# Performance work log

Hardware: AMD Instinct MI355X
Metric: run time of the kernel (lower is better)

## Reference

```python
import jax, jax.numpy as jnp
import numpy as np

C = 256   # d_model
L = 2     # num_decoder_layers
B = 4
H = 128
W = 128
WH = 8    # dec_win_h
WW = 16   # dec_win_w
EPS = 1e-5


def _gn(x, w, b):
    # GroupNorm with 1 group: normalize over (C,H,W) per sample, per-channel affine
    mu = jnp.mean(x, axis=(1, 2, 3), keepdims=True)
    var = jnp.mean((x - mu) ** 2, axis=(1, 2, 3), keepdims=True)
    xn = (x - mu) * jax.lax.rsqrt(var + EPS)
    return xn * w[:, None, None] + b[:, None, None]


def _conv1x1(x, w, b):
    # x: [B,C,H,W], w: [O,C], b: [O]
    return jnp.einsum('bchw,oc->bohw', x, w) + b[:, None, None]


def _avgpool3(x):
    # AvgPool2d(3, stride=1, padding=1, count_include_pad=False)
    dims = (1, 1, 3, 3)
    strides = (1, 1, 1, 1)
    pad = [(0, 0), (0, 0), (1, 1), (1, 1)]
    s = jax.lax.reduce_window(x, 0.0, jax.lax.add, dims, strides, pad)
    ones = jnp.ones((1, 1) + x.shape[2:], x.dtype)
    cnt = jax.lax.reduce_window(ones, 0.0, jax.lax.add, dims, strides, pad)
    return s / cnt


def _mix(x):
    # PoolFormer token mixer: avgpool(x) - x
    return _avgpool3(x) - x


def _win_part(x, wh, ww):
    # [B,C,H,W] -> [B*nWin, C, wh, ww]
    b, c, h, w = x.shape
    x = x.reshape(b, c, h // wh, wh, w // ww, ww)
    x = x.transpose(0, 2, 4, 1, 3, 5)
    return x.reshape(-1, c, wh, ww)


def _agp(tgt, mem, qw, qb, kw, kb, vw, vb):
    # AttentionGuidedPooling; NOTE: torch uses .view(B,-1,C) on [B,C,H,W],
    # a raw reshape (not a transpose) -- replicated faithfully here.
    bw, c, h, w = mem.shape
    n = h * w
    q = _conv1x1(tgt, qw, qb).reshape(bw, n, c)
    k = _conv1x1(mem, kw, kb).reshape(bw, n, c)
    v = _conv1x1(mem, vw, vb).reshape(bw, n, c)
    attn = jax.nn.softmax(jnp.einsum('bnc,bmc->bnm', q, k), axis=-1)
    out = jnp.einsum('bnm,bmc->bnc', attn, v)
    return out.reshape(bw, c, h, w)


def _layer(tgt, mem, p):
    (gn1_w, gn1_b, gn2_w, gn2_b, ls1, ls2, ls3,
     qw, qb, kw, kb, vw, vb, fc1_w, fc1_b, fc2_w, fc2_b) = p
    tgt2 = tgt + ls1[:, None, None] * _mix(_gn(tgt, gn1_w, gn1_b))
    guided = _agp(tgt, mem, qw, qb, kw, kb, vw, vb)
    tgt3 = tgt2 + guided
    tgt3 = tgt2 + ls2[:, None, None] * _mix(_gn(tgt3, gn1_w, gn1_b))
    h = _gn(tgt3, gn2_w, gn2_b)
    h = _conv1x1(h, fc1_w, fc1_b)
    h = jax.nn.gelu(h, approximate=False)  # torch nn.GELU default (erf)
    h = _conv1x1(h, fc2_w, fc2_b)
    return tgt3 + ls3[:, None, None] * h


def setup_inputs() -> dict:
    key = jax.random.key(0)
    ks = jax.random.split(key, 16)
    s = 0.02
    inp = {
        'src': jax.random.normal(ks[0], (B, C, H, W), jnp.float32),
        'query_feats': jax.random.normal(ks[1], (B, C, H, W), jnp.float32),
        'gn1_w': jnp.ones((L, C), jnp.float32),
        'gn1_b': jnp.zeros((L, C), jnp.float32),
        'gn2_w': jnp.ones((L, C), jnp.float32),
        'gn2_b': jnp.zeros((L, C), jnp.float32),
        'ls1': 1e-5 * jnp.ones((L, C), jnp.float32),
        'ls2': 1e-5 * jnp.ones((L, C), jnp.float32),
        'ls3': 1e-5 * jnp.ones((L, C), jnp.float32),
        'qw': s * jax.random.normal(ks[2], (L, C, C), jnp.float32),
        'qb': jnp.zeros((L, C), jnp.float32),
        'kw': s * jax.random.normal(ks[3], (L, C, C), jnp.float32),
        'kb': jnp.zeros((L, C), jnp.float32),
        'vw': s * jax.random.normal(ks[4], (L, C, C), jnp.float32),
        'vb': jnp.zeros((L, C), jnp.float32),
        'fc1_w': s * jax.random.normal(ks[5], (L, 2 * C, C), jnp.float32),
        'fc1_b': jnp.zeros((L, 2 * C), jnp.float32),
        'fc2_w': s * jax.random.normal(ks[6], (L, C, 2 * C), jnp.float32),
        'fc2_b': jnp.zeros((L, C), jnp.float32),
        'gnf_w': jnp.ones((C,), jnp.float32),
        'gnf_b': jnp.zeros((C,), jnp.float32),
    }
    return inp


def reference(src, query_feats, gn1_w, gn1_b, gn2_w, gn2_b, ls1, ls2, ls3,
              qw, qb, kw, kb, vw, vb, fc1_w, fc1_b, fc2_w, fc2_b, gnf_w, gnf_b):
    # pq_stride=8 -> div_ratio=1: memory windows same size as tgt windows
    mem = _win_part(src, WH, WW)
    out = _win_part(query_feats, WH, WW)
    for l in range(L):
        p = (gn1_w[l], gn1_b[l], gn2_w[l], gn2_b[l], ls1[l], ls2[l], ls3[l],
             qw[l], qb[l], kw[l], kb[l], vw[l], vb[l],
             fc1_w[l], fc1_b[l], fc2_w[l], fc2_b[l])
        out = _layer(out, mem, p)
    out = _gn(out, gnf_w, gnf_b)
    # window reverse -> [B, C, H, W] -> sequence [B, H*W, C]
    nwh, nww = H // WH, W // WW
    x = out.reshape(B, nwh, nww, C, WH, WW).transpose(0, 3, 1, 4, 2, 5)
    x = x.reshape(B, C, H * W)
    hs = jnp.swapaxes(x, 1, 2)[None]        # [1, B, N, C]
    return jnp.swapaxes(hs, 1, 2)           # [1, N, B, C]
```

## Files before the change

### kernel.cpp

```cpp
#include <hip/hip_runtime.h>
#include <hip/hip_bf16.h>

typedef __hip_bfloat16 bf16_t;
typedef short bf16x8 __attribute__((ext_vector_type(8)));
typedef float f32x4 __attribute__((ext_vector_type(4)));

__device__ __forceinline__ float bfr(unsigned short u) {
  return __uint_as_float(((unsigned int)u) << 16);
}
__device__ __forceinline__ float b2f(bf16_t h) { return __bfloat162float(h); }
__device__ __forceinline__ bf16_t f2b(float f) { return __float2bfloat16(f); }
__device__ __forceinline__ unsigned short f2bu(float f) {
  union { bf16_t h; unsigned short u; } cv; cv.h = __float2bfloat16(f); return cv.u;
}
__device__ __forceinline__ void unpk2(unsigned int u, float& a, float& b) {
  a = __uint_as_float(u << 16);
  b = __uint_as_float(u & 0xffff0000u);
}
__device__ __forceinline__ void ld8b(const bf16_t* p, float* o) {
  uint4 v = *(const uint4*)p;
  unpk2(v.x,o[0],o[1]); unpk2(v.y,o[2],o[3]); unpk2(v.z,o[4],o[5]); unpk2(v.w,o[6],o[7]);
}
__device__ __forceinline__ void unpk8(uint4 v, float* o) {
  unpk2(v.x,o[0],o[1]); unpk2(v.y,o[2],o[3]); unpk2(v.z,o[4],o[5]); unpk2(v.w,o[6],o[7]);
}
__device__ __forceinline__ int flag_of(const void* w) {
  return (*(const unsigned int*)w == 0x3F803F80u) ? 0 : 1;
}

typedef __attribute__((address_space(3))) void lds_t;
typedef __attribute__((address_space(1))) void glb_t;
__device__ __forceinline__ void gll16(const void* g, void* l) {
  __builtin_amdgcn_global_load_lds((glb_t*)g, (lds_t*)l, 16, 0, 0);
}

struct Srcs { const void* p[18]; };

__global__ __launch_bounds__(256)
void k_cvtall(Srcs a, bf16_t* __restrict__ PR) {
  const int ck = blockIdx.x*256 + threadIdx.x;
  if (ck >= 115520) return;
  constexpr int N8[18]  = {64,64,64,64,64,64,64,64,64,128,64,32,32,16384,16384,16384,32768,32768};
  constexpr int DOF[18] = {0,512,1024,1536,2048,2560,3072,3584,4096,4608,5632,6144,6400,8192,139264,270336,401408,663552};
  int s = 0, base = 0, doff = 0, cum = 0;
#pragma unroll
  for (int i = 0; i < 17; ++i) {
    cum += N8[i];
    if (ck >= cum) { s = i + 1; base = cum; doff = DOF[i + 1]; }
  }
  const int o8 = ck - base;
  const void* sp = a.p[s];
  const int fl = flag_of(a.p[0]);
  uint4 w;
  if (fl) {
    const float4* f = (const float4*)sp;
    float4 v0 = f[o8*2], v1 = f[o8*2+1];
    w.x = ((unsigned)f2bu(v0.y)<<16) | f2bu(v0.x);
    w.y = ((unsigned)f2bu(v0.w)<<16) | f2bu(v0.z);
    w.z = ((unsigned)f2bu(v1.y)<<16) | f2bu(v1.x);
    w.w = ((unsigned)f2bu(v1.w)<<16) | f2bu(v1.z);
  } else {
    w = ((const uint4*)sp)[o8];
  }
  *(uint4*)(PR + doff + o8*8) = w;
}

__global__ __launch_bounds__(256)
void k_xt2(const void* __restrict__ inA, bf16_t* __restrict__ outA,
           const void* __restrict__ inB, bf16_t* __restrict__ outB,
           const void* __restrict__ flagw) {
  __shared__ unsigned short L[128*130];
  const void* in = blockIdx.z ? inB : inA;
  bf16_t* out = blockIdx.z ? outB : outA;
  const int win = blockIdx.x, tile = blockIdx.y, tid = threadIdx.x;
  const int IC = tile << 7;
  const int fl = flag_of(flagw);
  const int b = win >> 7, whi = (win >> 3) & 15, wwi = win & 7;

  for (int i = 0; i < 8; ++i) {
    int idx = tid + (i<<8);
    int r = idx >> 4, ch = idx & 15;
    unsigned int w0, w1, w2, w3;
    int c = IC + r;
    int hq = ch >> 1, wq = (ch & 1) << 3;
    long gaddr = ((long)((b<<8) + c) << 14) + ((whi<<3) + hq)*128 + (wwi<<4) + wq;
    if (fl) {
      const float* gp = (const float*)in + gaddr;
      float4 aa = *(const float4*)gp, bb = *(const float4*)(gp+4);
      w0 = ((unsigned)f2bu(aa.y)<<16)|f2bu(aa.x); w1 = ((unsigned)f2bu(aa.w)<<16)|f2bu(aa.z);
      w2 = ((unsigned)f2bu(bb.y)<<16)|f2bu(bb.x); w3 = ((unsigned)f2bu(bb.w)<<16)|f2bu(bb.z);
    } else {
      uint4 v = *(const uint4*)((const bf16_t*)in + gaddr);
      w0 = v.x; w1 = v.y; w2 = v.z; w3 = v.w;
    }
    unsigned int* Lp = (unsigned int*)L;
    int u32o = (r*130 + (ch<<3)) >> 1;
    Lp[u32o+0] = w0; Lp[u32o+1] = w1; Lp[u32o+2] = w2; Lp[u32o+3] = w3;
  }
  __syncthreads();
  for (int i = 0; i < 8; ++i) {
    int idx = tid + (i<<8);
    int q = idx >> 4, ch = idx & 15;
    unsigned short pk[8];
#pragma unroll
    for (int j = 0; j < 8; ++j) pk[j] = L[((ch<<3) + j)*130 + q];
    *(uint4*)(out + (long)win*32768 + (long)q*256 + IC + (ch<<3)) = *(uint4*)pk;
  }
}

__global__ __launch_bounds__(256) void k_statsP(const bf16_t* __restrict__ X, float* __restrict__ st) {
  __shared__ float s1[256], s2[256];
  int w = blockIdx.x, tid = threadIdx.x;
  const bf16_t* x = X + ((long)w << 15);
  float a = 0.f, b = 0.f;
  for (int i = tid*8; i < 32768; i += 2048) {
    float t[8]; ld8b(x + i, t);
#pragma unroll
    for (int j = 0; j < 8; ++j) { a += t[j]; b += t[j]*t[j]; }
  }
  s1[tid] = a; s2[tid] = b;
  __syncthreads();
  for (int off = 128; off > 0; off >>= 1) {
    if (tid < off) { s1[tid] += s1[tid+off]; s2[tid] += s2[tid+off]; }
    __syncthreads();
  }
  if (tid == 0) {
    float mu = s1[0] * (1.0f/32768.0f);
    float var = s2[0] * (1.0f/32768.0f) - mu*mu;
    st[(w<<1)]   = mu;
    st[(w<<1)+1] = rsqrtf(var + 1e-5f);
  }
}

template<int GATH, int GN2>
__global__ __launch_bounds__(512, 4)
void k_poolf(const bf16_t* __restrict__ Xp, const bf16_t* __restrict__ Gc,
             bf16_t* __restrict__ Out,
             const bf16_t* __restrict__ lsv, const bf16_t* __restrict__ gw,
             bf16_t* __restrict__ G2,
             const bf16_t* __restrict__ g2w, const bf16_t* __restrict__ g2b) {
  __shared__ unsigned short L[32768];
  __shared__ float s1[8], s2[8];
  __shared__ float mr[2];
  const int win = blockIdx.x;
  const int tid = threadIdx.x;
  const long wb = (long)win << 15;
  float a = 0.f, b = 0.f;

#pragma unroll
  for (int i = 0; i < 8; ++i) {
    int k = (i<<9) + tid;
    int p = k >> 5, c8 = k & 31;
    uint4 v = *(const uint4*)(Xp + wb + (p<<8) + (c8<<3));
    *(uint4*)&L[(p<<8) + ((c8 ^ ((p>>3)&7))<<3)] = v;
    if (!GATH) {
      float t[8]; unpk8(v, t);
#pragma unroll
      for (int j = 0; j < 8; ++j) { a += t[j]; b += t[j]*t[j]; }
    }
  }
  if (GATH) {
    __syncthreads();
#pragma unroll
    for (int i = 0; i < 8; ++i) {
      int k = (i<<9) + tid;
      int c = k >> 4, p0 = (k & 15) << 3;
      uint4 gv = *(const uint4*)(Gc + wb + (c<<7) + p0);
      float g[8]; unpk8(gv, g);
      int ch = c >> 3, cl = c & 7;
      int sl = ((ch ^ ((p0>>3) & 7))<<3) + cl;
#pragma unroll
      for (int j = 0; j < 8; ++j) {
        int idx = ((p0 + j)<<8) + sl;
        float xx = bfr(L[idx]) + g[j];
        a += xx; b += xx*xx;
        L[idx] = f2bu(xx);
      }
    }
  }
#pragma unroll
  for (int d = 1; d < 64; d <<= 1) { a += __shfl_xor(a, d); b += __shfl_xor(b, d); }
  if ((tid & 63) == 0) { s1[tid>>6] = a; s2[tid>>6] = b; }
  __syncthreads();
  if (tid == 0) {
    float sa = 0.f, sb = 0.f;
#pragma unroll
    for (int i = 0; i < 8; ++i) { sa += s1[i]; sb += s2[i]; }
    float mu = sa * (1.0f/32768.0f);
    float var = sb * (1.0f/32768.0f) - mu*mu;
    mr[0] = mu; mr[1] = rsqrtf(var + 1e-5f);
  }
  __syncthreads();
  const float rstd = mr[1];
  const int c = tid & 255;
  const int hb = (tid >> 8) << 2;
  const int ch = c >> 3, cl = c & 7;
  const float scl = b2f(lsv[c]) * b2f(gw[c]) * rstd;
  float oa = 0.f, ob = 0.f;

  float rm1[16], r0[16], rp1[16];
#pragma unroll
  for (int ww = 0; ww < 16; ++ww) {
    int p0_ = (hb<<4) + ww;
    r0[ww] = bfr(L[(p0_<<8) + ((ch ^ ((p0_>>3)&7))<<3) + cl]);
    int p1_ = ((hb+1)<<4) + ww;
    rp1[ww] = bfr(L[(p1_<<8) + ((ch ^ ((p1_>>3)&7))<<3) + cl]);
  }
  if (hb > 0) {
#pragma unroll
    for (int ww = 0; ww < 16; ++ww) {
      int pm = ((hb-1)<<4) + ww;
      rm1[ww] = bfr(L[(pm<<8) + ((ch ^ ((pm>>3)&7))<<3) + cl]);
    }
  }
#pragma unroll
  for (int hl = 0; hl < 4; ++hl) {
    int h = hb + hl;
    float cs[16];
    float hc = 1.f + (h > 0 ? 1.f : 0.f) + (h < 7 ? 1.f : 0.f);
#pragma unroll
    for (int ww = 0; ww < 16; ++ww)
      cs[ww] = r0[ww] + (h > 0 ? rm1[ww] : 0.f) + (h < 7 ? rp1[ww] : 0.f);
#pragma unroll
    for (int ww = 0; ww < 16; ++ww) {
      float s = cs[ww];
      float wc = 1.f;
      if (ww > 0)  { s += cs[ww-1]; wc += 1.f; }
      if (ww < 15) { s += cs[ww+1]; wc += 1.f; }
      float avg = s / (hc * wc);
      float xx = r0[ww];
      int p = (h<<4) + ww;
      float base = xx;
      if (GATH) base = bfr(*(const unsigned short*)(Xp + wb + (p<<8) + c));
      float val = base + scl * (avg - xx);
      if (GN2) { oa += val; ob += val*val; }
      Out[wb + (p<<8) + c] = f2b(val);
    }
#pragma unroll
    for (int ww = 0; ww < 16; ++ww) { rm1[ww] = r0[ww]; r0[ww] = rp1[ww]; }
    if (hl < 3 && (h + 2) <= 7) {
      int hp = (h+2) << 4;
#pragma unroll
      for (int ww = 0; ww < 16; ++ww) {
        int p = hp + ww;
        rp1[ww] = bfr(L[(p<<8) + ((ch ^ ((p>>3)&7))<<3) + cl]);
      }
    }
  }
  if (GN2) {
#pragma unroll
    for (int d = 1; d < 64; d <<= 1) { oa += __shfl_xor(oa, d); ob += __shfl_xor(ob, d); }
    if ((tid & 63) == 0) { s1[tid>>6] = oa; s2[tid>>6] = ob; }
    __syncthreads();
    if (tid == 0) {
      float sa = 0.f, sb = 0.f;
#pragma unroll
      for (int i = 0; i < 8; ++i) { sa += s1[i]; sb += s2[i]; }
      float mu = sa * (1.0f/32768.0f);
      float var = sb * (1.0f/32768.0f) - mu*mu;
      mr[0] = mu; mr[1] = rsqrtf(var + 1e-5f);
    }
    __syncthreads();
    const float mu2 = mr[0], rs2 = mr[1];
#pragma unroll
    for (int i = 0; i < 8; ++i) {
      int k = (i<<9) + tid;
      int p = k >> 5, cv = k & 31;
      uint4 v = *(const uint4*)(Out + wb + (p<<8) + (cv<<3));
      float t[8]; unpk8(v, t);
      uint4 wv = *(const uint4*)(g2w + (cv<<3));
      uint4 bv = *(const uint4*)(g2b + (cv<<3));
      float wf[8], bf2[8]; unpk8(wv, wf); unpk8(bv, bf2);
      unsigned short pk[8];
#pragma unroll
      for (int j = 0; j < 8; ++j) pk[j] = f2bu((t[j]-mu2)*rs2*wf[j] + bf2[j]);
      *(uint4*)(G2 + wb + (p<<8) + (cv<<3)) = *(uint4*)pk;
    }
  }
}

#define GM_QKV  0
#define GM_NM   1
#define GM_GELU 2
#define GM_RES  3

template<int MODE>
__global__ __launch_bounds__(256, 2)
void k_gemm(const bf16_t* __restrict__ A, long sA, int lda,
            const bf16_t* __restrict__ B0, const bf16_t* __restrict__ B1,
            long sB, int ldb,
            bf16_t* __restrict__ Y, long sY, int ldy,
            const bf16_t* __restrict__ bias,
            const bf16_t* __restrict__ res, long sR,
            const bf16_t* __restrict__ ls,
            int K) {
  __shared__ uint4 LB[2048];
  unsigned short* As = (unsigned short*)LB;
  unsigned short* Bs = (unsigned short*)LB + 8192;
  unsigned short* E  = (unsigned short*)LB;
  const int win = blockIdx.x;
  const int tid = threadIdx.x;
  const int w = tid >> 6, lane = tid & 63;
  const int l15 = lane & 15, quad = lane >> 4;
  const int m0w = (w >> 1) << 6, n0w = (w & 1) << 6;

  int sel = 0, m0;
  const bf16_t *Ab, *Bb; bf16_t* Yb; const bf16_t* biasb = nullptr;
  if (MODE == GM_QKV) {
    sel = blockIdx.y >> 1; m0 = (blockIdx.y & 1) << 7;
    Ab = A + sel*131072 + (long)m0*lda;
    Bb = (sel ? B1 : B0) + (long)win*sB;
    Yb = Y + (long)sel*16777216 + (long)win*sY;
    biasb = bias + sel*512 + m0;
  } else {
    m0 = blockIdx.y << 7;
    Ab = A + (long)win*sA + (long)m0*lda;
    Bb = B0 + (long)win*sB;
    Yb = Y + (long)win*sY;
    if (bias) biasb = bias + m0;
  }
  const bool CT = (MODE == GM_QKV) && (sel < 2);

  int rr_[4], co_[4], lo_[4];
#pragma unroll
  for (int j = 0; j < 4; ++j) {
    int ck = (j<<8) + (w<<6) + lane;
    int r = ck >> 3;
    rr_[j] = r;
    co_[j] = ((ck & 7) ^ (r & 7)) << 3;
    lo_[j] = ((j<<8) + (w<<6)) << 3;
  }

  f32x4 acc[4][4];
#pragma unroll
  for (int i = 0; i < 4; ++i)
#pragma unroll
    for (int j = 0; j < 4; ++j) acc[i][j] = (f32x4){0.f,0.f,0.f,0.f};

  for (int k0 = 0; k0 < K; k0 += 64) {
#pragma unroll
    for (int j = 0; j < 4; ++j) {
      gll16(Ab + (long)rr_[j]*lda + k0 + co_[j], As + lo_[j]);
      gll16(Bb + (long)rr_[j]*ldb + k0 + co_[j], Bs + lo_[j]);
    }
    __syncthreads();
#pragma unroll
    for (int kk = 0; kk < 2; ++kk) {
      bf16x8 af[4], bv[4];
#pragma unroll
      for (int im = 0; im < 4; ++im) {
        int R = m0w + (im<<4) + l15;
        af[im] = *(const bf16x8*)&As[(R<<6) + ((((kk<<2)+quad) ^ (R&7))<<3)];
      }
#pragma unroll
      for (int in = 0; in < 4; ++in) {
        int R = n0w + (in<<4) + l15;
        bv[in] = *(const bf16x8*)&Bs[(R<<6) + ((((kk<<2)+quad) ^ (R&7))<<3)];
      }
      if (CT) {
#pragma unroll
        for (int im = 0; im < 4; ++im)
#pragma unroll
          for (int in = 0; in < 4; ++in)
            acc[im][in] = __builtin_amdgcn_mfma_f32_16x16x32_bf16(bv[in], af[im], acc[im][in], 0, 0, 0);
      } else {
#pragma unroll
        for (int im = 0; im < 4; ++im)
#pragma unroll
          for (int in = 0; in < 4; ++in)
            acc[im][in] = __builtin_amdgcn_mfma_f32_16x16x32_bf16(af[im], bv[in], acc[im][in], 0, 0, 0);
      }
    }
    __syncthreads();
  }

  if (MODE == GM_QKV && sel == 2) {
#pragma unroll
    for (int im = 0; im < 4; ++im) {
#pragma unroll
      for (int in = 0; in < 4; ++in) {
        f32x4 v = acc[im][in];
        int tok = n0w + (in<<4) + l15;
        int c0 = m0w + (im<<4) + (quad<<2);
        int u0 = c0 >> 1;
        float x0 = v[0] + b2f(biasb[c0]);
        float x1 = v[1] + b2f(biasb[c0+1]);
        float x2 = v[2] + b2f(biasb[c0+2]);
        float x3 = v[3] + b2f(biasb[c0+3]);
        int sl = (((u0>>3) ^ (tok&7))<<3) + (u0&7);
        *(unsigned int*)&E[(tok<<6) + sl]       = (unsigned)f2bu(x0) | ((unsigned)f2bu(x2)<<16);
        *(unsigned int*)&E[((128+tok)<<6) + sl] = (unsigned)f2bu(x1) | ((unsigned)f2bu(x3)<<16);
      }
    }
    __syncthreads();
#pragma unroll
    for (int i = 0; i < 8; ++i) {
      int ck = (i<<8) + tid;
      int cp = ck >> 3, u8 = ck & 7;
      uint4 v = *(const uint4*)&E[(cp<<6) + ((u8 ^ (cp&7))<<3)];
      *(uint4*)(Yb + (long)cp*128 + (m0>>1) + (u8<<3)) = v;
    }
    return;
  }

  if (CT) {
#pragma unroll
    for (int half = 0; half < 2; ++half) {
      if (m0w == (half<<6)) {
#pragma unroll
        for (int im = 0; im < 4; ++im) {
          int row = (im<<4) + l15;
          float bm = b2f(biasb[(half<<6) + row]);
#pragma unroll
          for (int in = 0; in < 4; ++in) {
            f32x4 v = acc[im][in];
            unsigned short pk[4];
#pragma unroll
            for (int r = 0; r < 4; ++r) pk[r] = f2bu(v[r] + bm);
            *(ushort4*)&E[row*136 + n0w + (in<<4) + (quad<<2)] = *(ushort4*)pk;
          }
        }
      }
      __syncthreads();
#pragma unroll
      for (int i = 0; i < 4; ++i) {
        int ck = (i<<8) + tid;
        int row = ck >> 4, c8 = (ck & 15) << 3;
        uint4 v = *(const uint4*)&E[row*136 + c8];
        *(uint4*)(Yb + (long)(m0 + (half<<6) + row)*ldy + c8) = v;
      }
      __syncthreads();
    }
    return;
  }

#pragma unroll
  for (int half = 0; half < 2; ++half) {
    if (n0w == (half<<6)) {
#pragma unroll
      for (int in = 0; in < 4; ++in) {
        int row = (in<<4) + l15;
#pragma unroll
        for (int im = 0; im < 4; ++im) {
          f32x4 v = acc[im][in];
          int mb = m0w + (im<<4) + (quad<<2);
          unsigned short pk[4];
#pragma unroll
          for (int r = 0; r < 4; ++r) {
            float x = v[r];
            if (MODE == GM_GELU || MODE == GM_RES) x += b2f(biasb[mb + r]);
            if (MODE == GM_GELU) x = 0.5f * x * (1.0f + erff(x * 0.70710678118654752f));
            pk[r] = f2bu(x);
          }
          *(ushort4*)&E[row*136 + mb] = *(ushort4*)pk;
        }
      }
    }
    __syncthreads();
#pragma unroll
    for (int i = 0; i < 4; ++i) {
      int ck = (i<<8) + tid;
      int rloc = ck >> 4, c8 = (ck & 15) << 3;
      long oadr = (long)((half<<6) + rloc)*ldy + m0 + c8;
      uint4 v = *(const uint4*)&E[rloc*136 + c8];
      if (MODE == GM_RES) {
        float t[8]; unpk8(v, t);
        uint4 rv = *(const uint4*)(res + (long)win*sR + oadr);
        float rf[8]; unpk8(rv, rf);
        uint4 lv = *(const uint4*)(ls + m0 + c8);
        float lf[8]; unpk8(lv, lf);
        unsigned short pk[8];
#pragma unroll
        for (int j = 0; j < 8; ++j) pk[j] = f2bu(rf[j] + lf[j]*t[j]);
        *(uint4*)(Yb + oadr) = *(uint4*)pk;
      } else {
        *(uint4*)(Yb + oadr) = v;
      }
    }
    __syncthreads();
  }
}

__global__ __launch_bounds__(256, 2)
void k_scores(const bf16_t* __restrict__ Kc, const bf16_t* __restrict__ Qc,
              bf16_t* __restrict__ P) {
  __shared__ uint4 LB[2048];
  __shared__ float red[2][2][128];
  unsigned short* As = (unsigned short*)LB;
  unsigned short* Bs = (unsigned short*)LB + 8192;
  const int win = blockIdx.x;
  const int tid = threadIdx.x;
  const int w = tid >> 6, lane = tid & 63;
  const int l15 = lane & 15, quad = lane >> 4;
  const int m0w = (w >> 1) << 6, n0w = (w & 1) << 6;
  const int wrow = w >> 1;
  const bf16_t* Ab = Kc + ((long)win << 15);
  const bf16_t* Bb = Qc + ((long)win << 15);

  int rr_[4], co_[4], lo_[4];
#pragma unroll
  for (int j = 0; j < 4; ++j) {
    int ck = (j<<8) + (w<<6) + lane;
    int r = ck >> 3;
    rr_[j] = r;
    co_[j] = ((ck & 7) ^ (r & 7)) << 3;
    lo_[j] = ((j<<8) + (w<<6)) << 3;
  }

  f32x4 acc[4][4];
#pragma unroll
  for (int i = 0; i < 4; ++i)
#pragma unroll
    for (int j = 0; j < 4; ++j) acc[i][j] = (f32x4){0.f,0.f,0.f,0.f};

  for (int k0 = 0; k0 < 256; k0 += 64) {
#pragma unroll
    for (int j = 0; j < 4; ++j) {
      gll16(Ab + (long)rr_[j]*256 + k0 + co_[j], As + lo_[j]);
      gll16(Bb + (long)rr_[j]*256 + k0 + co_[j], Bs + lo_[j]);
    }
    __syncthreads();
#pragma unroll
    for (int kk = 0; kk < 2; ++kk) {
      bf16x8 af[4], bv[4];
#pragma unroll
      for (int im = 0; im < 4; ++im) {
        int R = m0w + (im<<4) + l15;
        af[im] = *(const bf16x8*)&As[(R<<6) + ((((kk<<2)+quad) ^ (R&7))<<3)];
      }
#pragma unroll
      for (int in = 0; in < 4; ++in) {
        int R = n0w + (in<<4) + l15;
        bv[in] = *(const bf16x8*)&Bs[(R<<6) + ((((kk<<2)+quad) ^ (R&7))<<3)];
      }
#pragma unroll
      for (int im = 0; im < 4; ++im)
#pragma unroll
        for (int in = 0; in < 4; ++in)
          acc[im][in] = __builtin_amdgcn_mfma_f32_16x16x32_bf16(af[im], bv[in], acc[im][in], 0, 0, 0);
    }
    __syncthreads();
  }

  float mx[4];
#pragma unroll
  for (int in = 0; in < 4; ++in) {
    float m = -3.4e38f;
#pragma unroll
    for (int im = 0; im < 4; ++im)
#pragma unroll
      for (int r = 0; r < 4; ++r) m = fmaxf(m, acc[im][in][r]);
    m = fmaxf(m, __shfl_xor(m, 16));
    m = fmaxf(m, __shfl_xor(m, 32));
    mx[in] = m;
  }
  if (quad == 0) {
#pragma unroll
    for (int in = 0; in < 4; ++in) red[0][wrow][n0w + (in<<4) + l15] = mx[in];
  }
  __syncthreads();
  float fm[4];
#pragma unroll
  for (int in = 0; in < 4; ++in) {
    int t = n0w + (in<<4) + l15;
    fm[in] = fmaxf(red[0][0][t], red[0][1][t]);
  }
  float sm[4];
#pragma unroll
  for (int in = 0; in < 4; ++in) {
    float s = 0.f;
#pragma unroll
    for (int im = 0; im < 4; ++im)
#pragma unroll
      for (int r = 0; r < 4; ++r) {
        float e = __expf(acc[im][in][r] - fm[in]);
        acc[im][in][r] = e;
        s += e;
      }
    s += __shfl_xor(s, 16);
    s += __shfl_xor(s, 32);
    sm[in] = s;
  }
  if (quad == 0) {
#pragma unroll
    for (int in = 0; in < 4; ++in) red[1][wrow][n0w + (in<<4) + l15] = sm[in];
  }
  __syncthreads();
  bf16_t* Pw = P + ((long)win << 14);
#pragma unroll
  for (int in = 0; in < 4; ++in) {
    int t = n0w + (in<<4) + l15;
    float inv = 1.0f / (red[1][0][t] + red[1][1][t]);
#pragma unroll
    for (int im = 0; im < 4; ++im) {
      int u = m0w + (im<<4) + (quad<<2);
      unsigned short pk[4];
#pragma unroll
      for (int r = 0; r < 4; ++r) pk[r] = f2bu(acc[im][in][r] * inv);
      *(ushort4*)(Pw + t*128 + u) = *(ushort4*)pk;
    }
  }
}

__global__ __launch_bounds__(256)
void k_final(const bf16_t* __restrict__ Tp, const float* __restrict__ st,
             const bf16_t* __restrict__ gw, const bf16_t* __restrict__ gb,
             void* __restrict__ out, const void* __restrict__ flagw) {
  const int fl = flag_of(flagw);
  long k = (long)blockIdx.x*256 + threadIdx.x;
  int c8 = (int)(k & 31), p = (int)((k >> 5) & 127), win = (int)(k >> 12);
  float mu = st[win*2], rs = st[win*2+1];
  uint4 v = *(const uint4*)(Tp + (k<<3));
  float t[8]; unpk8(v, t);
  uint4 wv = *(const uint4*)(gw + (c8<<3));
  uint4 bv = *(const uint4*)(gb + (c8<<3));
  float wf[8], bf2[8]; unpk8(wv, wf); unpk8(bv, bf2);
  float o_[8];
#pragma unroll
  for (int j = 0; j < 8; ++j) o_[j] = (t[j] - mu) * rs * wf[j] + bf2[j];
  int b = win >> 7, whi = (win >> 3) & 15, wwi = win & 7;
  int n = ((whi<<3) + (p>>4)) * 128 + (wwi<<4) + (p & 15);
  long o = ((long)((n<<2) + b) << 8) + (c8<<3);
  if (fl) {
    float4 f0, f1;
    f0.x=o_[0]; f0.y=o_[1]; f0.z=o_[2]; f0.w=o_[3];
    f1.x=o_[4]; f1.y=o_[5]; f1.z=o_[6]; f1.w=o_[7];
    *(float4*)((float*)out + o)     = f0;
    *(float4*)((float*)out + o + 4) = f1;
  } else {
    unsigned short pk[8];
#pragma unroll
    for (int j = 0; j < 8; ++j) pk[j] = f2bu(o_[j]);
    *(uint4*)((bf16_t*)out + o) = *(uint4*)pk;
  }
}

extern "C" void kernel_launch(void* const* d_in, const int* in_sizes, int n_in,
                              void* d_out, int out_size, void* d_ws, size_t ws_size,
                              hipStream_t stream) {
  (void)in_sizes; (void)n_in; (void)out_size; (void)ws_size;
  const void* src   = d_in[0];
  const void* qfeat = d_in[1];

  bf16_t* W    = (bf16_t*)d_ws;
  bf16_t* Tp   = W;
  bf16_t* T2p  = W + 16777216;
  bf16_t* Sp   = W + 33554432;
  bf16_t* slA  = W + 50331648;
  bf16_t* KcGc = W + 67108864;
  bf16_t* Vc   = W + 83886080;
  bf16_t* Hp   = KcGc;
  bf16_t* P    = W + 100663296;
  bf16_t* PR   = W + 109051904;
  float*  ST   = (float*)(W + 110100480);
  float*  st0  = ST;

  bf16_t* gn1w = PR;
  bf16_t* gn2w = PR + 512;
  bf16_t* gn2b = PR + 1024;
  bf16_t* ls1  = PR + 1536;
  bf16_t* ls2  = PR + 2048;
  bf16_t* ls3  = PR + 2560;
  bf16_t* qb   = PR + 3072;
  bf16_t* f1b  = PR + 4608;
  bf16_t* f2bp = PR + 5632;
  bf16_t* gfw  = PR + 6144;
  bf16_t* gfb  = PR + 6400;
  bf16_t* qw   = PR + 8192;
  bf16_t* f1w  = PR + 401408;
  bf16_t* f2w  = PR + 663552;

  Srcs sa;
  const int map[18] = {2,4,5,6,7,8,10,12,14,16,18,19,20,9,11,13,15,17};
  for (int i = 0; i < 18; ++i) sa.p[i] = d_in[map[i]];
  k_cvtall<<<452, 256, 0, stream>>>(sa, PR);

  k_xt2<<<dim3(512,2,2), 256, 0, stream>>>(qfeat, Tp, src, Sp, d_in[2]);

  for (int l = 0; l < 2; ++l) {
    k_poolf<0,0><<<512, 512, 0, stream>>>(Tp, nullptr, T2p, ls1 + l*256, gn1w + l*256,
                                          nullptr, nullptr, nullptr);
    k_gemm<GM_QKV><<<dim3(512,6), 256, 0, stream>>>(
        qw + l*65536, 0, 256, Tp, Sp, 32768, 256, slA, 32768, 128,
        qb + l*256, nullptr, 0, nullptr, 256);
    k_scores<<<512, 256, 0, stream>>>(KcGc, slA, P);
    k_gemm<GM_NM><<<dim3(512,2), 256, 0, stream>>>(
        Vc, 32768, 128, P, nullptr, 16384, 128, KcGc, 32768, 256,
        nullptr, nullptr, 0, nullptr, 128);
    k_poolf<1,1><<<512, 512, 0, stream>>>(T2p, KcGc, Tp, ls2 + l*256, gn1w + l*256,
                                          slA, gn2w + l*256, gn2b + l*256);
    k_gemm<GM_GELU><<<dim3(512,4), 256, 0, stream>>>(
        f1w + l*131072, 0, 256, slA, nullptr, 32768, 256, Hp, 65536, 512,
        f1b + l*512, nullptr, 0, nullptr, 256);
    k_gemm<GM_RES><<<dim3(512,2), 256, 0, stream>>>(
        f2w + l*131072, 0, 512, Hp, nullptr, 65536, 512, Tp, 32768, 256,
        f2bp + l*256, Tp, 32768, ls3 + l*256, 512);
  }

  k_statsP<<<512, 256, 0, stream>>>(Tp, st0);
  k_final<<<8192, 256, 0, stream>>>(Tp, st0, gfw, gfb, d_out, d_in[2]);
}
```

Baseline: 739.7 us.

## Fuse final GroupNorm stats into last residual GEMM and restructure window transpose

Removes the separate k_statsP pass by having the last FC2 residual GEMM accumulate per-window sum and sum-of-squares with atomics, with k_final deriving mean and rstd from them. The stats buffer is zeroed inside the transpose kernel. That transpose is also rewritten so each block reads full 128-wide image rows, which gives more contiguous global loads, and uses an XOR-swizzled LDS layout in place of padding. The cost is atomic adds, an extra reduction in the GEMM epilogue, and changed float summation order.

```diff
diff --git a/kernel.cpp b/kernel.cpp
--- a/kernel.cpp
+++ b/kernel.cpp
@@ -68,67 +68,59 @@
 __global__ __launch_bounds__(256)
 void k_xt2(const void* __restrict__ inA, bf16_t* __restrict__ outA,
            const void* __restrict__ inB, bf16_t* __restrict__ outB,
-           const void* __restrict__ flagw) {
-  __shared__ unsigned short L[128*130];
+           const void* __restrict__ flagw, float* __restrict__ st0) {
+  __shared__ unsigned short L[16384];
+  unsigned int* Ld = (unsigned int*)L;
   const void* in = blockIdx.z ? inB : inA;
   bf16_t* out = blockIdx.z ? outB : outA;
-  const int win = blockIdx.x, tile = blockIdx.y, tid = threadIdx.x;
-  const int IC = tile << 7;
+  const int x = blockIdx.x;
+  const int b = x >> 7, whi = (x >> 3) & 15, hq = x & 7;
+  const int IC = blockIdx.y << 7;
+  const int tid = threadIdx.x;
   const int fl = flag_of(flagw);
-  const int b = win >> 7, whi = (win >> 3) & 15, wwi = win & 7;
-
-  for (int i = 0; i < 8; ++i) {
-    int idx = tid + (i<<8);
-    int r = idx >> 4, ch = idx & 15;
-    unsigned int w0, w1, w2, w3;
-    int c = IC + r;
-    int hq = ch >> 1, wq = (ch & 1) << 3;
-    long gaddr = ((long)((b<<8) + c) << 14) + ((whi<<3) + hq)*128 + (wwi<<4) + wq;
-    if (fl) {
-      const float* gp = (const float*)in + gaddr;
-      float4 aa = *(const float4*)gp, bb = *(const float4*)(gp+4);
-      w0 = ((unsigned)f2bu(aa.y)<<16)|f2bu(aa.x); w1 = ((unsigned)f2bu(aa.w)<<16)|f2bu(aa.z);
-      w2 = ((unsigned)f2bu(bb.y)<<16)|f2bu(bb.x); w3 = ((unsigned)f2bu(bb.w)<<16)|f2bu(bb.z);
-    } else {
-      uint4 v = *(const uint4*)((const bf16_t*)in + gaddr);
-      w0 = v.x; w1 = v.y; w2 = v.z; w3 = v.w;
-    }
-    unsigned int* Lp = (unsigned int*)L;
-    int u32o = (r*130 + (ch<<3)) >> 1;
-    Lp[u32o+0] = w0; Lp[u32o+1] = w1; Lp[u32o+2] = w2; Lp[u32o+3] = w3;
+  const int h = (whi << 3) + hq;
+
+  if (blockIdx.z == 0 && blockIdx.y == 0 && hq == 0 && tid < 16)
+    st0[(((b<<4) + whi)<<4) + tid] = 0.f;
+
+  if (fl) {
+    for (int i = 0; i < 16; ++i) {
+      int idx = (i<<8) + tid;
+      int r = idx >> 5, w4 = idx & 31;
+      long ga = ((long)((b<<8) + IC + r) << 14) + (h<<7) + (w4<<2);
+      float4 v = *(const float4*)((const float*)in + ga);
+      unsigned int d0 = ((unsigned)f2bu(v.y)<<16) | f2bu(v.x);
+      unsigned int d1 = ((unsigned)f2bu(v.w)<<16) | f2bu(v.z);
+      int s = (r >> 3) << 1;
+      int p0 = (r<<6) + ((w4<<1) ^ s);
+      Ld[p0] = d0; Ld[p0+1] = d1;
+    }
+  } else {
+    for (int i = 0; i < 8; ++i) {
+      int idx = (i<<8) + tid;
+      int r = idx >> 4, w8 = idx & 15;
+      long ga = ((long)((b<<8) + IC + r) << 14) + (h<<7) + (w8<<3);
+      uint4 v = *(const uint4*)((const bf16_t*)in + ga);
+      int s = (r >> 3) << 1;
+      int d0 = (r<<6) + (((w8<<2)    ) ^ s);
+      int d1 = (r<<6) + (((w8<<2) + 2) ^ s);
+      Ld[d0] = v.x; Ld[d0+1] = v.y;
+      Ld[d1] = v.z; Ld[d1+1] = v.w;
+    }
   }
   __syncthreads();
-  for (int i = 0; i < 8; ++i) {
-    int idx = tid + (i<<8);
-    int q = idx >> 4, ch = idx & 15;
+  const int ch16 = tid & 15, wl = tid >> 4;
+  const int p = (hq<<4) + wl;
+  const int s = ch16 << 1;
+  const int rbase = (ch16 << 3) << 7;
+  for (int wwi = 0; wwi < 8; ++wwi) {
+    int w = (wwi<<4) + wl;
+    int colu = (((w>>1) ^ s)<<1) + (w&1);
     unsigned short pk[8];
 #pragma unroll
-    for (int j = 0; j < 8; ++j) pk[j] = L[((ch<<3) + j)*130 + q];
-    *(uint4*)(out + (long)win*32768 + (long)q*256 + IC + (ch<<3)) = *(uint4*)pk;
-  }
-}
-
-__global__ __launch_bounds__(256) void k_statsP(const bf16_t* __restrict__ X, float* __restrict__ st) {
-  __shared__ float s1[256], s2[256];
-  int w = blockIdx.x, tid = threadIdx.x;
-  const bf16_t* x = X + ((long)w << 15);
-  float a = 0.f, b = 0.f;
-  for (int i = tid*8; i < 32768; i += 2048) {
-    float t[8]; ld8b(x + i, t);
-#pragma unroll
-    for (int j = 0; j < 8; ++j) { a += t[j]; b += t[j]*t[j]; }
-  }
-  s1[tid] = a; s2[tid] = b;
-  __syncthreads();
-  for (int off = 128; off > 0; off >>= 1) {
-    if (tid < off) { s1[tid] += s1[tid+off]; s2[tid] += s2[tid+off]; }
-    __syncthreads();
-  }
-  if (tid == 0) {
-    float mu = s1[0] * (1.0f/32768.0f);
-    float var = s2[0] * (1.0f/32768.0f) - mu*mu;
-    st[(w<<1)]   = mu;
-    st[(w<<1)+1] = rsqrtf(var + 1e-5f);
+    for (int j = 0; j < 8; ++j) pk[j] = L[rbase + (j<<7) + colu];
+    int win = (b<<7) + (whi<<3) + wwi;
+    *(uint4*)(out + (long)win*32768 + (p<<8) + IC + (ch16<<3)) = *(uint4*)pk;
   }
 }
 
@@ -293,7 +285,7 @@
             const bf16_t* __restrict__ bias,
             const bf16_t* __restrict__ res, long sR,
             const bf16_t* __restrict__ ls,
-            int K) {
+            int K, float* __restrict__ stp) {
   __shared__ uint4 LB[2048];
   unsigned short* As = (unsigned short*)LB;
   unsigned short* Bs = (unsigned short*)LB + 8192;
@@ -374,6 +366,8 @@
     __syncthreads();
   }
 
+  float oa = 0.f, ob = 0.f;
+
   if (MODE == GM_QKV && sel == 2) {
 #pragma unroll
     for (int im = 0; im < 4; ++im) {
@@ -471,13 +465,33 @@
         float lf[8]; unpk8(lv, lf);
         unsigned short pk[8];
 #pragma unroll
-        for (int j = 0; j < 8; ++j) pk[j] = f2bu(rf[j] + lf[j]*t[j]);
+        for (int j = 0; j < 8; ++j) {
+          pk[j] = f2bu(rf[j] + lf[j]*t[j]);
+          float vr = bfr(pk[j]);
+          oa += vr; ob += vr*vr;
+        }
         *(uint4*)(Yb + oadr) = *(uint4*)pk;
       } else {
         *(uint4*)(Yb + oadr) = v;
       }
     }
     __syncthreads();
+  }
+
+  if (MODE == GM_RES) {
+    if (stp) {
+#pragma unroll
+      for (int d = 1; d < 64; d <<= 1) { oa += __shfl_xor(oa, d); ob += __shfl_xor(ob, d); }
+      float* RS = (float*)LB;
+      if (lane == 0) { RS[w*2] = oa; RS[w*2+1] = ob; }
+      __syncthreads();
+      if (tid == 0) {
+        float sa = RS[0]+RS[2]+RS[4]+RS[6];
+        float sb = RS[1]+RS[3]+RS[5]+RS[7];
+        atomicAdd(&stp[win*2], sa);
+        atomicAdd(&stp[win*2+1], sb);
+      }
+    }
   }
 }
 
@@ -609,7 +623,9 @@
   const int fl = flag_of(flagw);
   long k = (long)blockIdx.x*256 + threadIdx.x;
   int c8 = (int)(k & 31), p = (int)((k >> 5) & 127), win = (int)(k >> 12);
-  float mu = st[win*2], rs = st[win*2+1];
+  float sa = st[win*2], sb = st[win*2+1];
+  float mu = sa * (1.0f/32768.0f);
+  float rs = rsqrtf(sb * (1.0f/32768.0f) - mu*mu + 1e-5f);
   uint4 v = *(const uint4*)(Tp + (k<<3));
   float t[8]; unpk8(v, t);
   uint4 wv = *(const uint4*)(gw + (c8<<3));
@@ -675,28 +691,27 @@
   for (int i = 0; i < 18; ++i) sa.p[i] = d_in[map[i]];
   k_cvtall<<<452, 256, 0, stream>>>(sa, PR);
 
-  k_xt2<<<dim3(512,2,2), 256, 0, stream>>>(qfeat, Tp, src, Sp, d_in[2]);
+  k_xt2<<<dim3(512,2,2), 256, 0, stream>>>(qfeat, Tp, src, Sp, d_in[2], st0);
 
   for (int l = 0; l < 2; ++l) {
     k_poolf<0,0><<<512, 512, 0, stream>>>(Tp, nullptr, T2p, ls1 + l*256, gn1w + l*256,
                                           nullptr, nullptr, nullptr);
     k_gemm<GM_QKV><<<dim3(512,6), 256, 0, stream>>>(
         qw + l*65536, 0, 256, Tp, Sp, 32768, 256, slA, 32768, 128,
-        qb + l*256, nullptr, 0, nullptr, 256);
+        qb + l*256, nullptr, 0, nullptr, 256, nullptr);
     k_scores<<<512, 256, 0, stream>>>(KcGc, slA, P);
     k_gemm<GM_NM><<<dim3(512,2), 256, 0, stream>>>(
         Vc, 32768, 128, P, nullptr, 16384, 128, KcGc, 32768, 256,
-        nullptr, nullptr, 0, nullptr, 128);
+        nullptr, nullptr, 0, nullptr, 128, nullptr);
     k_poolf<1,1><<<512, 512, 0, stream>>>(T2p, KcGc, Tp, ls2 + l*256, gn1w + l*256,
                                           slA, gn2w + l*256, gn2b + l*256);
     k_gemm<GM_GELU><<<dim3(512,4), 256, 0, stream>>>(
         f1w + l*131072, 0, 256, slA, nullptr, 32768, 256, Hp, 65536, 512,
-        f1b + l*512, nullptr, 0, nullptr, 256);
+        f1b + l*512, nullptr, 0, nullptr, 256, nullptr);
     k_gemm<GM_RES><<<dim3(512,2), 256, 0, stream>>>(
         f2w + l*131072, 0, 512, Hp, nullptr, 65536, 512, Tp, 32768, 256,
-        f2bp + l*256, Tp, 32768, ls3 + l*256, 512);
-  }
-
-  k_statsP<<<512, 256, 0, stream>>>(Tp, st0);
+        f2bp + l*256, Tp, 32768, ls3 + l*256, 512, (l == 1) ? st0 : nullptr);
+  }
+
   k_final<<<8192, 256, 0, stream>>>(Tp, st0, gfw, gfb, d_out, d_in[2]);
 }
```

After: 917.9 us. 24.1% more time.
